# Kernel optimization log

Hardware: AMD Instinct MI355X
Metric: run time of the kernel (lower is better)

## Reference

```python
import jax, jax.numpy as jnp
import numpy as np


def setup_inputs() -> dict:
    key = jax.random.key(0)
    ks = jax.random.split(key, 9)
    B, C, H, W = 16, 512, 64, 64
    C8 = C // 8
    s_in = 1.0 / np.sqrt(C)
    s_out = 1.0 / np.sqrt(C8)
    return {
        "x": jax.random.normal(ks[0], (B, C, H, W), dtype=jnp.float32),
        "Wq": jax.random.normal(ks[1], (C8, C), dtype=jnp.float32) * s_in,
        "bq": jax.random.normal(ks[2], (C8,), dtype=jnp.float32) * s_in,
        "Wk": jax.random.normal(ks[3], (C8, C), dtype=jnp.float32) * s_in,
        "bk": jax.random.normal(ks[4], (C8,), dtype=jnp.float32) * s_in,
        "Wv": jax.random.normal(ks[5], (C8, C), dtype=jnp.float32) * s_in,
        "bv": jax.random.normal(ks[6], (C8,), dtype=jnp.float32) * s_in,
        "Wo": jax.random.normal(ks[7], (C, C8), dtype=jnp.float32) * s_out,
        "bo": jax.random.normal(ks[8], (C,), dtype=jnp.float32) * s_out,
    }


def reference(x, Wq, bq, Wk, bk, Wv, bv, Wo, bo):
    B, C, H, W = x.shape
    N = H * W
    xf = x.reshape(B, C, N)  # 1x1 conv == channel matmul over flattened spatial
    q = jnp.einsum("oc,bcn->bon", Wq, xf) + bq[None, :, None]  # [B, C8, N]
    k = jnp.einsum("oc,bcn->bon", Wk, xf) + bk[None, :, None]
    v = jnp.einsum("oc,bcn->bon", Wv, xf) + bv[None, :, None]
    energy = jnp.einsum("bcn,bdn->bcd", q, k)  # [B, C8, C8] channel attention
    attn = jax.nn.softmax(energy, axis=-1)
    out = jnp.einsum("bcd,bdn->bcn", attn, v)  # [B, C8, N]
    out = jnp.einsum("oc,bcn->bon", Wo, out) + bo[None, :, None]  # [B, C, N]
    return out.reshape(B, C, H, W)
```

## Files before the change

kernel.cpp:

```cpp
#include <hip/hip_runtime.h>
#include <hip/hip_bf16.h>
#include <cstdint>

#define B_SZ 16
#define C_IN 512
#define C8   64
#define NSP  4096
#define QR   192

typedef __attribute__((ext_vector_type(8))) short s8v;
typedef __attribute__((ext_vector_type(4))) float f4v;

__device__ __forceinline__ void split_bf16(float x, unsigned short& h, unsigned short& l) {
    unsigned int u = __float_as_uint(x);
    h = (unsigned short)(u >> 16);
    float r = x - __uint_as_float(u & 0xffff0000u);
    l = (unsigned short)(__float_as_uint(r) >> 16);
}

__device__ __forceinline__ void split8(const float* v, s8v& h, s8v& l) {
#pragma unroll
    for (int j = 0; j < 8; ++j) {
        unsigned short hh, ll;
        split_bf16(v[j], hh, ll);
        h[j] = (short)hh; l[j] = (short)ll;
    }
}

__device__ __forceinline__ int eqaddr(int row, int n) {
    return row * 128 + ((((n >> 2) ^ ((row & 7) << 2)) << 2) | (n & 3));
}

__global__ __launch_bounds__(256) void k_convW(
    const float* __restrict__ Wq, const float* __restrict__ Wk,
    const float* __restrict__ Wv,
    unsigned short* __restrict__ whi, unsigned short* __restrict__ wlo)
{
    const int o = blockIdx.x;
    const float* src = (o < 64)  ? (Wq + (size_t)o * C_IN)
                     : (o < 128) ? (Wk + (size_t)(o - 64) * C_IN)
                                 : (Wv + (size_t)(o - 128) * C_IN);
    for (int c = threadIdx.x; c < C_IN; c += 256) {
        unsigned short h, l;
        split_bf16(src[c], h, l);
        whi[(size_t)o * C_IN + c] = h;
        wlo[(size_t)o * C_IN + c] = l;
    }
}

__global__ __launch_bounds__(512, 4) void k_qkv_en(
    const float* __restrict__ x,
    const unsigned short* __restrict__ whi, const unsigned short* __restrict__ wlo,
    const float* __restrict__ bq, const float* __restrict__ bk,
    const float* __restrict__ bv,
    float* __restrict__ v, float* __restrict__ part)
{
    __shared__ __align__(16) unsigned char smem[65536];
    unsigned short* as_h = (unsigned short*)smem;
    unsigned short* as_l = as_h + QR * 32;
    unsigned short* xs_h = as_l + QR * 32;
    unsigned short* xs_l = xs_h + 128 * 32;
    float* eq = (float*)smem;

    const int b  = blockIdx.y;
    const int s  = blockIdx.x;
    const int n0 = s * 128;
    const int t  = threadIdx.x;
    const int w  = t >> 6, l = t & 63;
    const int wm = w >> 1, wn = w & 1;
    const int lm = l & 15, lq = l >> 4;
    const int slot = ((lq ^ (l & 3)) << 3);

    const int nB = t & 127, kgB = t >> 7;
    const int slotB = ((kgB ^ (nB & 3)) << 3);

    const int mW = t >> 2, kgW = t & 3;
    const int dstW0 = mW * 32 + ((kgW ^ (mW & 3)) << 3);
    const size_t sW0 = (size_t)mW * C_IN + kgW * 8;

    f4v acc[3][4];
#pragma unroll
    for (int i = 0; i < 3; ++i)
#pragma unroll
        for (int j = 0; j < 4; ++j) acc[i][j] = (f4v)0.f;

    const float* xcol = x + (size_t)b * C_IN * NSP + n0 + nB;
    float xr[8];
    auto loadB = [&](int K0) {
        const float* s_ = xcol + (size_t)(K0 + kgB * 8) * NSP;
#pragma unroll
        for (int j = 0; j < 8; ++j) xr[j] = s_[(size_t)j * NSP];
    };
    loadB(0);

    for (int it = 0; it < 16; ++it) {
        const int k0 = it * 32;
        __syncthreads();
        s8v hv, lv;
        {
            unsigned short h, lo_;
#pragma unroll
            for (int j = 0; j < 8; ++j) {
                split_bf16(xr[j], h, lo_);
                hv[j] = (short)h; lv[j] = (short)lo_;
            }
        }
        if (it < 15) loadB(k0 + 32);
        s8v wh0 = *(const s8v*)&whi[sW0 + k0];
        s8v wl0 = *(const s8v*)&wlo[sW0 + k0];
        s8v wh1, wl1;
        if (t < 256) {
            wh1 = *(const s8v*)&whi[sW0 + 65536 + k0];
            wl1 = *(const s8v*)&wlo[sW0 + 65536 + k0];
        }
        *(s8v*)&xs_h[nB * 32 + slotB] = hv;
        *(s8v*)&xs_l[nB * 32 + slotB] = lv;
        *(s8v*)&as_h[dstW0] = wh0;
        *(s8v*)&as_l[dstW0] = wl0;
        if (t < 256) {
            *(s8v*)&as_h[dstW0 + 4096] = wh1;
            *(s8v*)&as_l[dstW0 + 4096] = wl1;
        }
        __syncthreads();
        s8v ah[3], al[3], bh[4], bl[4];
#pragma unroll
        for (int fm = 0; fm < 3; ++fm) {
            const int m = wm * 48 + fm * 16 + lm;
            ah[fm] = *(const s8v*)&as_h[m * 32 + slot];
            al[fm] = *(const s8v*)&as_l[m * 32 + slot];
        }
#pragma unroll
        for (int fn = 0; fn < 4; ++fn) {
            const int n = wn * 64 + fn * 16 + lm;
            bh[fn] = *(const s8v*)&xs_h[n * 32 + slot];
            bl[fn] = *(const s8v*)&xs_l[n * 32 + slot];
        }
#pragma unroll
        for (int fm = 0; fm < 3; ++fm)
#pragma unroll
            for (int fn = 0; fn < 4; ++fn) {
                acc[fm][fn] = __builtin_amdgcn_mfma_f32_16x16x32_bf16(
                    ah[fm], bh[fn], acc[fm][fn], 0, 0, 0);
                acc[fm][fn] = __builtin_amdgcn_mfma_f32_16x16x32_bf16(
                    ah[fm], bl[fn], acc[fm][fn], 0, 0, 0);
                acc[fm][fn] = __builtin_amdgcn_mfma_f32_16x16x32_bf16(
                    al[fm], bh[fn], acc[fm][fn], 0, 0, 0);
            }
    }

    __syncthreads();
#pragma unroll
    for (int fm = 0; fm < 3; ++fm) {
        const int row0f = wm * 48 + fm * 16;
        const int rbase = row0f + lq * 4;
        if (row0f >= 128) {
#pragma unroll
            for (int fn = 0; fn < 4; ++fn) {
                const int n = wn * 64 + fn * 16 + lm;
                float* dst = v + ((size_t)b * 64 + (rbase - 128)) * NSP + n0 + n;
#pragma unroll
                for (int r = 0; r < 4; ++r)
                    dst[(size_t)r * NSP] = acc[fm][fn][r] + bv[rbase - 128 + r];
            }
        } else {
            const float* barr = (row0f < 64) ? bq : bk;
            const int boff = rbase & 63;
#pragma unroll
            for (int fn = 0; fn < 4; ++fn) {
                const int n = wn * 64 + fn * 16 + lm;
#pragma unroll
                for (int r = 0; r < 4; ++r)
                    eq[eqaddr(rbase + r, n)] = acc[fm][fn][r] + barr[boff + r];
            }
        }
    }
    __syncthreads();

    const int fc = w >> 1, fd0 = (w & 1) * 2;
    f4v e0 = (f4v)0.f, e1 = (f4v)0.f;
#pragma unroll
    for (int ks = 0; ks < 4; ++ks) {
        const int nf = ks * 32 + lq * 8;
        float qa[8];
        {
            const int a0 = eqaddr(fc * 16 + lm, nf);
            *(float4*)&qa[0] = *(const float4*)&eq[a0];
            *(float4*)&qa[4] = *(const float4*)&eq[a0 + 4];
        }
        s8v qh, ql_;
        split8(qa, qh, ql_);
        float ka[8];
        {
            const int a0 = eqaddr(64 + fd0 * 16 + lm, nf);
            *(float4*)&ka[0] = *(const float4*)&eq[a0];
            *(float4*)&ka[4] = *(const float4*)&eq[a0 + 4];
        }
        s8v kh, kl_;
        split8(ka, kh, kl_);
        e0 = __builtin_amdgcn_mfma_f32_16x16x32_bf16(qh, kh,  e0, 0, 0, 0);
        e0 = __builtin_amdgcn_mfma_f32_16x16x32_bf16(qh, kl_, e0, 0, 0, 0);
        e0 = __builtin_amdgcn_mfma_f32_16x16x32_bf16(ql_, kh, e0, 0, 0, 0);
        {
            const int a0 = eqaddr(64 + (fd0 + 1) * 16 + lm, nf);
            *(float4*)&ka[0] = *(const float4*)&eq[a0];
            *(float4*)&ka[4] = *(const float4*)&eq[a0 + 4];
        }
        split8(ka, kh, kl_);
        e1 = __builtin_amdgcn_mfma_f32_16x16x32_bf16(qh, kh,  e1, 0, 0, 0);
        e1 = __builtin_amdgcn_mfma_f32_16x16x32_bf16(qh, kl_, e1, 0, 0, 0);
        e1 = __builtin_amdgcn_mfma_f32_16x16x32_bf16(ql_, kh, e1, 0, 0, 0);
    }
    float* pb = part + ((size_t)b * 32 + s) * 4096;
#pragma unroll
    for (int r = 0; r < 4; ++r) {
        const int c = fc * 16 + lq * 4 + r;
        pb[c * 64 + fd0 * 16 + lm]        = e0[r];
        pb[c * 64 + (fd0 + 1) * 16 + lm]  = e1[r];
    }
}

__global__ __launch_bounds__(256) void k_softmax(
    const float* __restrict__ part, float* __restrict__ attn)
{
    __shared__ float red[4][64];
    const int cRow = blockIdx.x, b = blockIdx.y;
    const int t = threadIdx.x, d = t & 63, sg = t >> 6;
    const float* p = part + (size_t)b * 32 * 4096 + cRow * 64 + d;
    float s = 0.f;
#pragma unroll
    for (int i = 0; i < 8; ++i) s += p[(size_t)(sg * 8 + i) * 4096];
    red[sg][d] = s;
    __syncthreads();
    if (t < 64) {
        float v = red[0][d] + red[1][d] + red[2][d] + red[3][d];
        float m = v;
#pragma unroll
        for (int off = 32; off; off >>= 1) m = fmaxf(m, __shfl_xor(m, off));
        float e = __expf(v - m);
        float sum = e;
#pragma unroll
        for (int off = 32; off; off >>= 1) sum += __shfl_xor(sum, off);
        attn[((size_t)b * 64 + cRow) * 64 + d] = e / sum;
    }
}

__global__ __launch_bounds__(256) void k_woattn(
    const float* __restrict__ Wo, const float* __restrict__ attn,
    unsigned short* __restrict__ mhi, unsigned short* __restrict__ mlo)
{
    __shared__ float wosT[64][68];
    __shared__ float as[64][68];
    const int b  = blockIdx.y;
    const int o0 = blockIdx.x * 64;
    const int t  = threadIdx.x;
    const int td = t & 15, to = t >> 4;
#pragma unroll
    for (int i = 0; i < 4; ++i) {
        int idx = t + 256 * i;
        int r = idx >> 4, q4 = idx & 15;
        float4 w = *reinterpret_cast<const float4*>(
            Wo + (size_t)(o0 + r) * 64 + q4 * 4);
        wosT[q4 * 4 + 0][r] = w.x; wosT[q4 * 4 + 1][r] = w.y;
        wosT[q4 * 4 + 2][r] = w.z; wosT[q4 * 4 + 3][r] = w.w;
        float4 a = *reinterpret_cast<const float4*>(
            attn + ((size_t)b * 64 + r) * 64 + q4 * 4);
        *reinterpret_cast<float4*>(&as[r][q4 * 4]) = a;
    }
    __syncthreads();
    float acc[4][4];
#pragma unroll
    for (int i = 0; i < 4; ++i)
#pragma unroll
        for (int j = 0; j < 4; ++j) acc[i][j] = 0.f;
#pragma unroll 8
    for (int kk = 0; kk < 64; ++kk) {
        float4 wv = *reinterpret_cast<const float4*>(&wosT[kk][to * 4]);
        float4 av = *reinterpret_cast<const float4*>(&as[kk][td * 4]);
        const float wr[4] = {wv.x, wv.y, wv.z, wv.w};
        const float ar[4] = {av.x, av.y, av.z, av.w};
#pragma unroll
        for (int i = 0; i < 4; ++i)
#pragma unroll
            for (int j = 0; j < 4; ++j)
                acc[i][j] = fmaf(wr[i], ar[j], acc[i][j]);
    }
#pragma unroll
    for (int i = 0; i < 4; ++i) {
        unsigned short h[4], lo4[4];
#pragma unroll
        for (int j = 0; j < 4; ++j) split_bf16(acc[i][j], h[j], lo4[j]);
        const size_t base = ((size_t)b * 512 + o0 + to * 4 + i) * 64 + td * 4;
        uint2 hp, lp;
        hp.x = (unsigned)h[0]   | ((unsigned)h[1]   << 16);
        hp.y = (unsigned)h[2]   | ((unsigned)h[3]   << 16);
        lp.x = (unsigned)lo4[0] | ((unsigned)lo4[1] << 16);
        lp.y = (unsigned)lo4[2] | ((unsigned)lo4[3] << 16);
        *reinterpret_cast<uint2*>(&mhi[base]) = hp;
        *reinterpret_cast<uint2*>(&mlo[base]) = lp;
    }
}

__global__ __launch_bounds__(512, 2) void k_out2(
    const float* __restrict__ v,
    const unsigned short* __restrict__ mhi, const unsigned short* __restrict__ mlo,
    const float* __restrict__ bo, float* __restrict__ out)
{
    __shared__ unsigned short vsT_h[64 * 64];
    __shared__ unsigned short vsT_l[64 * 64];
    const int b  = blockIdx.y;
    const int n0 = blockIdx.x * 64;
    const int t  = threadIdx.x;
    const int w  = t >> 6, l = t & 63;
    const int lm = l & 15, lq = l >> 4;

#pragma unroll
    for (int i = 0; i < 8; ++i) {
        const int d = w * 8 + i;
        const float xv = v[((size_t)b * 64 + d) * NSP + n0 + l];
        unsigned short h, lo_;
        split_bf16(xv, h, lo_);
        const int addr = l * 64 + ((((d >> 3) ^ (l & 7))) << 3) + (d & 7);
        vsT_h[addr] = h;
        vsT_l[addr] = lo_;
    }
    __syncthreads();

    f4v acc[4][4];
#pragma unroll
    for (int i = 0; i < 4; ++i)
#pragma unroll
        for (int j = 0; j < 4; ++j) acc[i][j] = (f4v)0.f;

    const int obase = w * 64;
#pragma unroll
    for (int ks = 0; ks < 2; ++ks) {
        s8v bh[4], bl[4];
#pragma unroll
        for (int fn = 0; fn < 4; ++fn) {
            const int n = fn * 16 + lm;
            const int addr = n * 64 + ((((ks * 4 + lq) ^ (n & 7))) << 3);
            bh[fn] = *(const s8v*)&vsT_h[addr];
            bl[fn] = *(const s8v*)&vsT_l[addr];
        }
#pragma unroll
        for (int fo = 0; fo < 4; ++fo) {
            const int o = obase + fo * 16 + lm;
            const size_t moff = ((size_t)b * 512 + o) * 64 + ks * 32 + lq * 8;
            s8v ah  = *(const s8v*)&mhi[moff];
            s8v al_ = *(const s8v*)&mlo[moff];
#pragma unroll
            for (int fn = 0; fn < 4; ++fn) {
                acc[fo][fn] = __builtin_amdgcn_mfma_f32_16x16x32_bf16(
                    ah, bh[fn], acc[fo][fn], 0, 0, 0);
                acc[fo][fn] = __builtin_amdgcn_mfma_f32_16x16x32_bf16(
                    ah, bl[fn], acc[fo][fn], 0, 0, 0);
                acc[fo][fn] = __builtin_amdgcn_mfma_f32_16x16x32_bf16(
                    al_, bh[fn], acc[fo][fn], 0, 0, 0);
            }
        }
    }

#pragma unroll
    for (int fo = 0; fo < 4; ++fo) {
        const int orow = obase + fo * 16 + lq * 4;
#pragma unroll
        for (int fn = 0; fn < 4; ++fn) {
            const int nc = n0 + fn * 16 + lm;
            float* dst = out + ((size_t)b * 512 + orow) * NSP + nc;
#pragma unroll
            for (int r = 0; r < 4; ++r)
                dst[(size_t)r * NSP] = acc[fo][fn][r] + bo[orow + r];
        }
    }
}

extern "C" void kernel_launch(void* const* d_in, const int* in_sizes, int n_in,
                              void* d_out, int out_size, void* d_ws, size_t ws_size,
                              hipStream_t stream)
{
    const float* x  = (const float*)d_in[0];
    const float* Wq = (const float*)d_in[1];
    const float* bq = (const float*)d_in[2];
    const float* Wk = (const float*)d_in[3];
    const float* bk = (const float*)d_in[4];
    const float* Wv = (const float*)d_in[5];
    const float* bv = (const float*)d_in[6];
    const float* Wo = (const float*)d_in[7];
    const float* bo = (const float*)d_in[8];
    float* out = (float*)d_out;

    float* ws   = (float*)d_ws;
    float* v    = ws;
    float* part = v    + (size_t)B_SZ * 64 * NSP;
    float* attn = part + (size_t)B_SZ * 32 * 64 * 64;
    unsigned short* mhi = (unsigned short*)(attn + (size_t)B_SZ * 64 * 64);
    unsigned short* mlo = mhi + (size_t)B_SZ * 512 * 64;
    unsigned short* whi = mlo + (size_t)B_SZ * 512 * 64;
    unsigned short* wlo = whi + (size_t)QR * C_IN;

    k_convW  <<<dim3(QR),      256, 0, stream>>>(Wq, Wk, Wv, whi, wlo);
    k_qkv_en <<<dim3(32, B_SZ), 512, 0, stream>>>(x, whi, wlo, bq, bk, bv, v, part);
    k_softmax<<<dim3(64, B_SZ), 256, 0, stream>>>(part, attn);
    k_woattn <<<dim3(8, B_SZ),  256, 0, stream>>>(Wo, attn, mhi, mlo);
    k_out2   <<<dim3(64, B_SZ), 512, 0, stream>>>(v, mhi, mlo, bo, out);
}
```

Baseline: 293.7 us.

## Fuse weight split into QKV kernel and softmax into Wo-attn kernel

```diff
diff --git a/kernel.cpp b/kernel.cpp
--- a/kernel.cpp
+++ b/kernel.cpp
@@ -31,26 +31,10 @@
     return row * 128 + ((((n >> 2) ^ ((row & 7) << 2)) << 2) | (n & 3));
 }
 
-__global__ __launch_bounds__(256) void k_convW(
+__global__ __launch_bounds__(512, 4) void k_qkv_en(
+    const float* __restrict__ x,
     const float* __restrict__ Wq, const float* __restrict__ Wk,
     const float* __restrict__ Wv,
-    unsigned short* __restrict__ whi, unsigned short* __restrict__ wlo)
-{
-    const int o = blockIdx.x;
-    const float* src = (o < 64)  ? (Wq + (size_t)o * C_IN)
-                     : (o < 128) ? (Wk + (size_t)(o - 64) * C_IN)
-                                 : (Wv + (size_t)(o - 128) * C_IN);
-    for (int c = threadIdx.x; c < C_IN; c += 256) {
-        unsigned short h, l;
-        split_bf16(src[c], h, l);
-        whi[(size_t)o * C_IN + c] = h;
-        wlo[(size_t)o * C_IN + c] = l;
-    }
-}
-
-__global__ __launch_bounds__(512, 4) void k_qkv_en(
-    const float* __restrict__ x,
-    const unsigned short* __restrict__ whi, const unsigned short* __restrict__ wlo,
     const float* __restrict__ bq, const float* __restrict__ bk,
     const float* __restrict__ bv,
     float* __restrict__ v, float* __restrict__ part)
@@ -74,9 +58,11 @@
     const int nB = t & 127, kgB = t >> 7;
     const int slotB = ((kgB ^ (nB & 3)) << 3);
 
-    const int mW = t >> 2, kgW = t & 3;
-    const int dstW0 = mW * 32 + ((kgW ^ (mW & 3)) << 3);
-    const size_t sW0 = (size_t)mW * C_IN + kgW * 8;
+    const int m0 = t >> 2, kg0 = t & 3;
+    const float* wr0 = ((m0 < 64) ? (Wq + (size_t)m0 * C_IN)
+                                  : (Wk + (size_t)(m0 - 64) * C_IN)) + kg0 * 8;
+    const float* wr1 = Wv + (size_t)m0 * C_IN + kg0 * 8;
+    const int dst0 = m0 * 32 + ((kg0 ^ (m0 & 3)) << 3);
 
     f4v acc[3][4];
 #pragma unroll
@@ -106,20 +92,25 @@
             }
         }
         if (it < 15) loadB(k0 + 32);
-        s8v wh0 = *(const s8v*)&whi[sW0 + k0];
-        s8v wl0 = *(const s8v*)&wlo[sW0 + k0];
-        s8v wh1, wl1;
+        float wv0[8], wv1[8];
+        *(float4*)&wv0[0] = *(const float4*)(wr0 + k0);
+        *(float4*)&wv0[4] = *(const float4*)(wr0 + k0 + 4);
         if (t < 256) {
-            wh1 = *(const s8v*)&whi[sW0 + 65536 + k0];
-            wl1 = *(const s8v*)&wlo[sW0 + 65536 + k0];
+            *(float4*)&wv1[0] = *(const float4*)(wr1 + k0);
+            *(float4*)&wv1[4] = *(const float4*)(wr1 + k0 + 4);
         }
         *(s8v*)&xs_h[nB * 32 + slotB] = hv;
         *(s8v*)&xs_l[nB * 32 + slotB] = lv;
-        *(s8v*)&as_h[dstW0] = wh0;
-        *(s8v*)&as_l[dstW0] = wl0;
-        if (t < 256) {
-            *(s8v*)&as_h[dstW0 + 4096] = wh1;
-            *(s8v*)&as_l[dstW0 + 4096] = wl1;
+        {
+            s8v wh, wl;
+            split8(wv0, wh, wl);
+            *(s8v*)&as_h[dst0] = wh;
+            *(s8v*)&as_l[dst0] = wl;
+            if (t < 256) {
+                split8(wv1, wh, wl);
+                *(s8v*)&as_h[dst0 + 4096] = wh;
+                *(s8v*)&as_l[dst0 + 4096] = wl;
+            }
         }
         __syncthreads();
         s8v ah[3], al[3], bh[4], bl[4];
@@ -219,54 +210,56 @@
     }
 }
 
-__global__ __launch_bounds__(256) void k_softmax(
-    const float* __restrict__ part, float* __restrict__ attn)
-{
-    __shared__ float red[4][64];
-    const int cRow = blockIdx.x, b = blockIdx.y;
-    const int t = threadIdx.x, d = t & 63, sg = t >> 6;
-    const float* p = part + (size_t)b * 32 * 4096 + cRow * 64 + d;
-    float s = 0.f;
-#pragma unroll
-    for (int i = 0; i < 8; ++i) s += p[(size_t)(sg * 8 + i) * 4096];
-    red[sg][d] = s;
-    __syncthreads();
-    if (t < 64) {
-        float v = red[0][d] + red[1][d] + red[2][d] + red[3][d];
-        float m = v;
-#pragma unroll
-        for (int off = 32; off; off >>= 1) m = fmaxf(m, __shfl_xor(m, off));
-        float e = __expf(v - m);
-        float sum = e;
-#pragma unroll
-        for (int off = 32; off; off >>= 1) sum += __shfl_xor(sum, off);
-        attn[((size_t)b * 64 + cRow) * 64 + d] = e / sum;
-    }
-}
-
-__global__ __launch_bounds__(256) void k_woattn(
-    const float* __restrict__ Wo, const float* __restrict__ attn,
+__global__ __launch_bounds__(256) void k_sm_wo(
+    const float* __restrict__ part, const float* __restrict__ Wo,
     unsigned short* __restrict__ mhi, unsigned short* __restrict__ mlo)
 {
+    __shared__ float es[64][65];
     __shared__ float wosT[64][68];
-    __shared__ float as[64][68];
     const int b  = blockIdx.y;
     const int o0 = blockIdx.x * 64;
     const int t  = threadIdx.x;
     const int td = t & 15, to = t >> 4;
+
 #pragma unroll
     for (int i = 0; i < 4; ++i) {
         int idx = t + 256 * i;
         int r = idx >> 4, q4 = idx & 15;
-        float4 w = *reinterpret_cast<const float4*>(
+        float4 wv = *reinterpret_cast<const float4*>(
             Wo + (size_t)(o0 + r) * 64 + q4 * 4);
-        wosT[q4 * 4 + 0][r] = w.x; wosT[q4 * 4 + 1][r] = w.y;
-        wosT[q4 * 4 + 2][r] = w.z; wosT[q4 * 4 + 3][r] = w.w;
-        float4 a = *reinterpret_cast<const float4*>(
-            attn + ((size_t)b * 64 + r) * 64 + q4 * 4);
-        *reinterpret_cast<float4*>(&as[r][q4 * 4]) = a;
-    }
-    __syncthreads();
+        wosT[q4 * 4 + 0][r] = wv.x; wosT[q4 * 4 + 1][r] = wv.y;
+        wosT[q4 * 4 + 2][r] = wv.z; wosT[q4 * 4 + 3][r] = wv.w;
+    }
+
+    const float* p = part + (size_t)b * 32 * 4096;
+#pragma unroll
+    for (int i = 0; i < 16; ++i) {
+        int idx = t + 256 * i;
+        float sum = 0.f;
+#pragma unroll 8
+        for (int s = 0; s < 32; ++s) sum += p[(size_t)s * 4096 + idx];
+        es[idx >> 6][idx & 63] = sum;
+    }
+    __syncthreads();
+
+    {
+        const int g = t >> 6, d = t & 63;
+#pragma unroll
+        for (int j = 0; j < 16; ++j) {
+            const int r = g + 4 * j;
+            float vv = es[r][d];
+            float m = vv;
+#pragma unroll
+            for (int off = 32; off; off >>= 1) m = fmaxf(m, __shfl_xor(m, off));
+            float e = __expf(vv - m);
+            float sum = e;
+#pragma unroll
+            for (int off = 32; off; off >>= 1) sum += __shfl_xor(sum, off);
+            es[r][d] = e / sum;
+        }
+    }
+    __syncthreads();
+
     float acc[4][4];
 #pragma unroll
     for (int i = 0; i < 4; ++i)
@@ -275,7 +268,7 @@
 #pragma unroll 8
     for (int kk = 0; kk < 64; ++kk) {
         float4 wv = *reinterpret_cast<const float4*>(&wosT[kk][to * 4]);
-        float4 av = *reinterpret_cast<const float4*>(&as[kk][td * 4]);
+        float4 av = *reinterpret_cast<const float4*>(&es[kk][td * 4]);
         const float wr[4] = {wv.x, wv.y, wv.z, wv.w};
         const float ar[4] = {av.x, av.y, av.z, av.w};
 #pragma unroll
@@ -392,15 +385,10 @@
     float* ws   = (float*)d_ws;
     float* v    = ws;
     float* part = v    + (size_t)B_SZ * 64 * NSP;
-    float* attn = part + (size_t)B_SZ * 32 * 64 * 64;
-    unsigned short* mhi = (unsigned short*)(attn + (size_t)B_SZ * 64 * 64);
+    unsigned short* mhi = (unsigned short*)(part + (size_t)B_SZ * 32 * 64 * 64);
     unsigned short* mlo = mhi + (size_t)B_SZ * 512 * 64;
-    unsigned short* whi = mlo + (size_t)B_SZ * 512 * 64;
-    unsigned short* wlo = whi + (size_t)QR * C_IN;
-
-    k_convW  <<<dim3(QR),      256, 0, stream>>>(Wq, Wk, Wv, whi, wlo);
-    k_qkv_en <<<dim3(32, B_SZ), 512, 0, stream>>>(x, whi, wlo, bq, bk, bv, v, part);
-    k_softmax<<<dim3(64, B_SZ), 256, 0, stream>>>(part, attn);
-    k_woattn <<<dim3(8, B_SZ),  256, 0, stream>>>(Wo, attn, mhi, mlo);
-    k_out2   <<<dim3(64, B_SZ), 512, 0, stream>>>(v, mhi, mlo, bo, out);
-}
+
+    k_qkv_en<<<dim3(32, B_SZ), 512, 0, stream>>>(x, Wq, Wk, Wv, bq, bk, bv, v, part);
+    k_sm_wo <<<dim3(8, B_SZ),  256, 0, stream>>>(part, Wo, mhi, mlo);
+    k_out2  <<<dim3(64, B_SZ), 512, 0, stream>>>(v, mhi, mlo, bo, out);
+}
```

New measurement: 318.9 us. 8.6% more time.
